# Performance work log

Hardware: AMD Instinct MI355X
Metric: run time of the kernel (lower is better)

## Reference

```python
import jax, jax.numpy as jnp
import numpy as np

U, I, D, OUT = 8192, 16384, 64, 64

def setup_inputs() -> dict:
    key = jax.random.key(0)
    k1, k2, k3, k4 = jax.random.split(key, 4)
    user_emb = jax.random.normal(k1, (U, D), dtype=jnp.float32)
    item_emb = jax.random.normal(k2, (I, D), dtype=jnp.float32)
    attention_weight = jax.random.normal(k3, (D, OUT), dtype=jnp.float32) * (1.0 / np.sqrt(D))
    adj_matrix = jax.random.randint(k4, (U, I), 0, 2, dtype=jnp.int32)
    return {"user_emb": user_emb, "item_emb": item_emb,
            "attention_weight": attention_weight, "adj_matrix": adj_matrix}

def reference(user_emb, item_emb, attention_weight, adj_matrix):
    # score[u,i] = <user_emb[u], item_emb[i]>  (torch.inner)
    score = jnp.einsum('ud,id->ui', user_emb, item_emb)
    # mask non-edges to 0 (NOT -inf, faithful to torch.where(adj>0, score, 0))
    score = jnp.where(adj_matrix > 0, score, 0.0)
    score = jax.nn.softmax(score, axis=1)
    # flag == True path: aggregate items into users, then project
    output = score @ item_emb          # [U, D]
    output = output @ attention_weight  # [U, OUT]
    return output
```

## Files before the change

### kernel.cpp

```cpp
#include <hip/hip_runtime.h>
#include <hip/hip_bf16.h>
#include <math.h>

#define U_N   8192
#define I_N   16384
#define D_N   64
#define OUT_N 64
#define BN    32
#define NCH   8
#define ITERS 64
#define VN_ST 72
#define VT_ST 40

typedef _Float16 half8  __attribute__((ext_vector_type(8)));
typedef short    bf16x8 __attribute__((ext_vector_type(8)));
typedef short    bf16x4 __attribute__((ext_vector_type(4)));
typedef float    f32x4  __attribute__((ext_vector_type(4)));
typedef int      int4v  __attribute__((ext_vector_type(4)));

static __device__ __forceinline__ unsigned short f2bf(float f) {
    union { __hip_bfloat16 h; unsigned short u; } cv;
    cv.h = __float2bfloat16(f);
    return cv.u;
}
static __device__ __forceinline__ float fast_exp2(float x) {
#if __has_builtin(__builtin_amdgcn_exp2f)
    return __builtin_amdgcn_exp2f(x);
#else
    return __expf(x * 0.6931471805599453f);
#endif
}
static __device__ __forceinline__ bf16x4 pack4(float a, float b, float c2, float d) {
    union { unsigned u[2]; bf16x4 h; } x;
#if __has_builtin(__builtin_amdgcn_perm)
    x.u[0] = __builtin_amdgcn_perm(__float_as_uint(b), __float_as_uint(a), 0x07060302u);
    x.u[1] = __builtin_amdgcn_perm(__float_as_uint(d), __float_as_uint(c2), 0x07060302u);
#else
    x.u[0] = (__float_as_uint(b) & 0xffff0000u) | (__float_as_uint(a) >> 16);
    x.u[1] = (__float_as_uint(d) & 0xffff0000u) | (__float_as_uint(c2) >> 16);
#endif
    return x.h;
}
static __device__ __forceinline__ void bar() {
    asm volatile("s_waitcnt lgkmcnt(0)\n\ts_barrier" ::: "memory");
}
static __device__ __forceinline__ f32x4 pv_mfma(bf16x4 a, bf16x4 b, f32x4 c) {
#if __has_builtin(__builtin_amdgcn_mfma_f32_16x16x16bf16_1k)
    return __builtin_amdgcn_mfma_f32_16x16x16bf16_1k(a, b, c, 0, 0, 0);
#else
    f32x4 d;
    asm volatile("v_mfma_f32_16x16x16_bf16 %0, %1, %2, %3"
                 : "=v"(d) : "v"(a), "v"(b), "v"(c));
    return d;
#endif
}

__global__ __launch_bounds__(256)
void prep_items(const float* __restrict__ item,
                _Float16* __restrict__ itemH,
                unsigned short* __restrict__ itemTt)
{
    const int i = blockIdx.x * 256 + threadIdx.x;
    const float* src = item + (size_t)i * D_N;
    f32x4 v[16];
    #pragma unroll
    for (int j = 0; j < 16; ++j) v[j] = *(const f32x4*)(src + 4 * j);

    #pragma unroll
    for (int j = 0; j < 8; ++j) {
        half8 h;
        #pragma unroll
        for (int k = 0; k < 4; ++k) { h[k] = (_Float16)v[2*j][k]; h[4+k] = (_Float16)v[2*j+1][k]; }
        *(half8*)&itemH[(size_t)i * D_N + 8 * j] = h;
    }
    const int il    = i & 31;
    const int islot = 8 * ((il & 15) >> 2) + ((il >> 4) << 2) + (il & 3);
    const size_t tb = (size_t)(i >> 5) * (D_N * 32) + islot;
    #pragma unroll
    for (int d = 0; d < 64; ++d)
        itemTt[tb + (size_t)d * 32] = f2bf(v[d >> 2][d & 3]);
}

#define DECL_SET(S) \
    int4v adj##S##a, adj##S##b; \
    half8 vn##S; bf16x8 vt##S;

#define LOAD_ADJ(S, tidx) do { \
    const size_t o_ = (size_t)(tidx) * BN; \
    adj##S##a = *(const int4v*)&adjq[o_];      \
    adj##S##b = *(const int4v*)&adjq[o_ + 16]; \
} while (0)

#define LOAD_TILE(S, tidx) do { \
    const size_t o_ = (size_t)(tidx) * BN; \
    vn##S = *(const half8*)&itemH[(ibase0 + o_ + (t >> 3)) * D_N + (t & 7) * 8]; \
    vt##S = *(const bf16x8*)&itemTt[((ibase0 + o_) >> 5) * (D_N * 32) \
                                    + (size_t)(t >> 2) * 32 + (t & 3) * 8]; \
} while (0)

#define COMMIT(S, bufw) do { \
    *(half8*)&Vn[bufw][(t >> 3) * VN_ST + (t & 7) * 8] = vn##S; \
    *(bf16x8*)&Vt[bufw][(t >> 2) * VT_ST + (t & 3) * 8] = vt##S; \
} while (0)

#define COMPUTE_REST(S, bufr) do { \
    half8 a00 = *(const half8*)&Vn[bufr][(c)      * VN_ST      + q * 8]; \
    half8 a01 = *(const half8*)&Vn[bufr][(c)      * VN_ST + 32 + q * 8]; \
    half8 a10 = *(const half8*)&Vn[bufr][(16 + c) * VN_ST      + q * 8]; \
    half8 a11 = *(const half8*)&Vn[bufr][(16 + c) * VN_ST + 32 + q * 8]; \
    bf16x8 w0 = *(const bf16x8*)&Vt[bufr][(c)      * VT_ST + 8 * q]; \
    bf16x8 w1 = *(const bf16x8*)&Vt[bufr][(16 + c) * VT_ST + 8 * q]; \
    bf16x8 w2 = *(const bf16x8*)&Vt[bufr][(32 + c) * VT_ST + 8 * q]; \
    bf16x8 w3 = *(const bf16x8*)&Vt[bufr][(48 + c) * VT_ST + 8 * q]; \
    f32x4 T0 = (f32x4){0.f,0.f,0.f,0.f}; \
    f32x4 T1 = (f32x4){0.f,0.f,0.f,0.f}; \
    T0 = __builtin_amdgcn_mfma_f32_16x16x32_f16(a00, ufrag0, T0, 0, 0, 0); \
    T0 = __builtin_amdgcn_mfma_f32_16x16x32_f16(a01, ufrag1, T0, 0, 0, 0); \
    T1 = __builtin_amdgcn_mfma_f32_16x16x32_f16(a10, ufrag0, T1, 0, 0, 0); \
    T1 = __builtin_amdgcn_mfma_f32_16x16x32_f16(a11, ufrag1, T1, 0, 0, 0); \
    const float e0_ = fast_exp2((adj##S##a[0] != 0) ? T0[0] : 0.0f); \
    const float e1_ = fast_exp2((adj##S##a[1] != 0) ? T0[1] : 0.0f); \
    const float e2_ = fast_exp2((adj##S##a[2] != 0) ? T0[2] : 0.0f); \
    const float e3_ = fast_exp2((adj##S##a[3] != 0) ? T0[3] : 0.0f); \
    const float f0_ = fast_exp2((adj##S##b[0] != 0) ? T1[0] : 0.0f); \
    const float f1_ = fast_exp2((adj##S##b[1] != 0) ? T1[1] : 0.0f); \
    const float f2_ = fast_exp2((adj##S##b[2] != 0) ? T1[2] : 0.0f); \
    const float f3_ = fast_exp2((adj##S##b[3] != 0) ? T1[3] : 0.0f); \
    lc += ((e0_ + e1_) + (e2_ + e3_)) + ((f0_ + f1_) + (f2_ + f3_)); \
    bf16x4 p0 = pack4(e0_, e1_, e2_, e3_); \
    bf16x4 p1 = pack4(f0_, f1_, f2_, f3_); \
    bf16x4 lo0 = __builtin_shufflevector(w0, w0, 0, 1, 2, 3); \
    bf16x4 hi0 = __builtin_shufflevector(w0, w0, 4, 5, 6, 7); \
    bf16x4 lo1 = __builtin_shufflevector(w1, w1, 0, 1, 2, 3); \
    bf16x4 hi1 = __builtin_shufflevector(w1, w1, 4, 5, 6, 7); \
    bf16x4 lo2 = __builtin_shufflevector(w2, w2, 0, 1, 2, 3); \
    bf16x4 hi2 = __builtin_shufflevector(w2, w2, 4, 5, 6, 7); \
    bf16x4 lo3 = __builtin_shufflevector(w3, w3, 0, 1, 2, 3); \
    bf16x4 hi3 = __builtin_shufflevector(w3, w3, 4, 5, 6, 7); \
    O0 = pv_mfma(p0, lo0, O0);  O0 = pv_mfma(p1, hi0, O0); \
    O1 = pv_mfma(p0, lo1, O1);  O1 = pv_mfma(p1, hi1, O1); \
    O2 = pv_mfma(p0, lo2, O2);  O2 = pv_mfma(p1, hi2, O2); \
    O3 = pv_mfma(p0, lo3, O3);  O3 = pv_mfma(p1, hi3, O3); \
} while (0)

__global__ __launch_bounds__(256, 4)
void atten_main(const float* __restrict__ user_emb,
                const _Float16* __restrict__ itemH,
                const unsigned short* __restrict__ itemTt,
                const int*   __restrict__ adj,
                float* __restrict__ wsO,
                float* __restrict__ wsL)
{
    __shared__ _Float16 Vn[2][BN * VN_ST];
    __shared__ short    Vt[2][D_N * VT_ST];

    const int ch   = blockIdx.x;
    const int ub   = blockIdx.y;
    const int t    = threadIdx.x;
    const int w    = t >> 6;
    const int lane = t & 63;
    const int c    = lane & 15;
    const int q    = lane >> 4;

    const int    urow0  = ub * 64 + w * 16;
    const size_t ibase0 = (size_t)ch * (I_N / NCH);

    half8 ufrag0, ufrag1;
    {
        const float* up = user_emb + (size_t)(urow0 + c) * D_N + q * 8;
        const float s = 1.44269504088896f;
        f32x4 a0 = *(const f32x4*)(up);
        f32x4 b0 = *(const f32x4*)(up + 4);
        f32x4 a1 = *(const f32x4*)(up + 32);
        f32x4 b1 = *(const f32x4*)(up + 36);
        #pragma unroll
        for (int j = 0; j < 4; ++j) {
            ufrag0[j] = (_Float16)(a0[j] * s); ufrag0[4 + j] = (_Float16)(b0[j] * s);
            ufrag1[j] = (_Float16)(a1[j] * s); ufrag1[4 + j] = (_Float16)(b1[j] * s);
        }
    }

    f32x4 O0 = (f32x4){0.f,0.f,0.f,0.f};
    f32x4 O1 = O0, O2 = O0, O3 = O0;
    float lc = 0.f;

    const int* adjq = adj + (size_t)(urow0 + c) * I_N + ibase0 + 4 * q;

    DECL_SET(A)
    DECL_SET(B)

    LOAD_TILE(A, 0); LOAD_ADJ(A, 0);
    LOAD_TILE(B, 1); LOAD_ADJ(B, 1);
    COMMIT(A, 0);
    LOAD_TILE(A, 2);
    bar();

    for (int k = 0; k < ITERS; k += 2) {
        {
            COMMIT(B, 1);
            LOAD_TILE(B, (k + 3 < ITERS) ? k + 3 : ITERS - 1);
            COMPUTE_REST(A, 0);
            LOAD_ADJ(A, (k + 2 < ITERS) ? k + 2 : ITERS - 1);
            bar();
        }
        {
            COMMIT(A, 0);
            LOAD_TILE(A, (k + 4 < ITERS) ? k + 4 : ITERS - 1);
            COMPUTE_REST(B, 1);
            LOAD_ADJ(B, (k + 3 < ITERS) ? k + 3 : ITERS - 1);
            bar();
        }
    }

    lc += __shfl_xor(lc, 16);
    lc += __shfl_xor(lc, 32);

    {
        float* d0 = wsO + ((size_t)ch * U_N + urow0 + 4 * q + 0) * D_N;
        float* d1 = wsO + ((size_t)ch * U_N + urow0 + 4 * q + 1) * D_N;
        float* d2 = wsO + ((size_t)ch * U_N + urow0 + 4 * q + 2) * D_N;
        float* d3 = wsO + ((size_t)ch * U_N + urow0 + 4 * q + 3) * D_N;
        d0[c] = O0[0]; d0[16 + c] = O1[0]; d0[32 + c] = O2[0]; d0[48 + c] = O3[0];
        d1[c] = O0[1]; d1[16 + c] = O1[1]; d1[32 + c] = O2[1]; d1[48 + c] = O3[1];
        d2[c] = O0[2]; d2[16 + c] = O1[2]; d2[32 + c] = O2[2]; d2[48 + c] = O3[2];
        d3[c] = O0[3]; d3[16 + c] = O1[3]; d3[32 + c] = O2[3]; d3[48 + c] = O3[3];
    }
    if (q == 0)
        wsL[(size_t)ch * U_N + urow0 + c] = lc;
}

__global__ __launch_bounds__(256)
void atten_combine(const float* __restrict__ wsO,
                   const float* __restrict__ wsL,
                   const float* __restrict__ attw,
                   float* __restrict__ out,
                   int nch)
{
    __shared__ float inv[64];
    __shared__ float agg[64][68];
    __shared__ float Wl[64][68];

    const int t  = threadIdx.x;
    const int u0 = blockIdx.x * 64;

    {
        const int d = t >> 2, o0 = (t & 3) * 16;
        const float* src = attw + d * OUT_N + o0;
        #pragma unroll
        for (int j = 0; j < 4; ++j)
            *(f32x4*)&Wl[d][o0 + 4 * j] = *(const f32x4*)(src + 4 * j);
    }
    if (t < 64) {
        float L = 0.f;
        for (int cc = 0; cc < nch; ++cc) L += wsL[(size_t)cc * U_N + u0 + t];
        inv[t] = 1.0f / L;
    }
    __syncthreads();

    {
        const int ul = t >> 2, d0 = (t & 3) * 16;
        const int u = u0 + ul;
        f32x4 a4[4];
        #pragma unroll
        for (int j = 0; j < 4; ++j) a4[j] = (f32x4){0.f, 0.f, 0.f, 0.f};
        for (int cc = 0; cc < nch; ++cc) {
            const float* src = wsO + ((size_t)cc * U_N + u) * D_N + d0;
            #pragma unroll
            for (int j = 0; j < 4; ++j) a4[j] += *(const f32x4*)(src + 4 * j);
        }
        const float s = inv[ul];
        #pragma unroll
        for (int j = 0; j < 4; ++j)
            *(f32x4*)&agg[ul][d0 + 4 * j] = a4[j] * s;
    }
    __syncthreads();

    {
        const int ul = t >> 2, o0 = (t & 3) * 16;
        f32x4 acc[4];
        #pragma unroll
        for (int j = 0; j < 4; ++j) acc[j] = (f32x4){0.f, 0.f, 0.f, 0.f};
        for (int d = 0; d < 64; ++d) {
            const float av = agg[ul][d];
            #pragma unroll
            for (int j = 0; j < 4; ++j) {
                f32x4 wv = *(const f32x4*)&Wl[d][o0 + 4 * j];
                acc[j] += wv * av;
            }
        }
        float* dst = out + (size_t)(u0 + ul) * OUT_N + o0;
        #pragma unroll
        for (int j = 0; j < 4; ++j)
            *(f32x4*)(dst + 4 * j) = acc[j];
    }
}

extern "C" void kernel_launch(void* const* d_in, const int* in_sizes, int n_in,
                              void* d_out, int out_size, void* d_ws, size_t ws_size,
                              hipStream_t stream)
{
    const float* user_emb = (const float*)d_in[0];
    const float* item_emb = (const float*)d_in[1];
    const float* attw     = (const float*)d_in[2];
    const int*   adj      = (const int*)d_in[3];
    float* out = (float*)d_out;

    float*          wsO    = (float*)d_ws;
    float*          wsL    = wsO + (size_t)NCH * U_N * D_N;
    _Float16*       itemH  = (_Float16*)(wsL + (size_t)NCH * U_N);
    unsigned short* itemTt = (unsigned short*)(itemH + (size_t)I_N * D_N);

    prep_items<<<dim3(I_N / 256), 256, 0, stream>>>(item_emb, itemH, itemTt);
    atten_main<<<dim3(NCH, U_N / 64), 256, 0, stream>>>(user_emb, itemH, itemTt, adj,
                                                        wsO, wsL);
    atten_combine<<<dim3(U_N / 64), 256, 0, stream>>>(wsO, wsL, attw, out, NCH);
}
```

Baseline: 728.4 us.

## Process two user row groups per wave to reuse item tiles

Each wave now handles 32 user rows (two 16-row groups 64 apart) instead of 16, so every item tile staged in shared memory feeds twice as many MFMAs and the grid halves along the user dimension. This cuts item-tile global and LDS traffic per unit of work, but raises register pressure, so the occupancy hint drops from 4 to 3 blocks per CU. The prep kernel is also split across four threads per item to reduce per-thread register use and improve parallelism. The adjacency stream, which dominates bandwidth, is unchanged.

```diff
diff --git a/kernel.cpp b/kernel.cpp
--- a/kernel.cpp
+++ b/kernel.cpp
@@ -7,6 +7,7 @@
 #define D_N   64
 #define OUT_N 64
 #define BN    32
+#define BM    128
 #define NCH   8
 #define ITERS 64
 #define VN_ST 72
@@ -60,35 +61,46 @@
                 _Float16* __restrict__ itemH,
                 unsigned short* __restrict__ itemTt)
 {
-    const int i = blockIdx.x * 256 + threadIdx.x;
-    const float* src = item + (size_t)i * D_N;
-    f32x4 v[16];
+    const int tid = blockIdx.x * 256 + threadIdx.x;
+    const int i   = tid >> 2;
+    const int g   = tid & 3;
+    const float* src = item + (size_t)i * D_N + g * 16;
+    f32x4 v0 = *(const f32x4*)(src);
+    f32x4 v1 = *(const f32x4*)(src + 4);
+    f32x4 v2 = *(const f32x4*)(src + 8);
+    f32x4 v3 = *(const f32x4*)(src + 12);
+
+    half8 h0, h1;
     #pragma unroll
-    for (int j = 0; j < 16; ++j) v[j] = *(const f32x4*)(src + 4 * j);
-
-    #pragma unroll
-    for (int j = 0; j < 8; ++j) {
-        half8 h;
-        #pragma unroll
-        for (int k = 0; k < 4; ++k) { h[k] = (_Float16)v[2*j][k]; h[4+k] = (_Float16)v[2*j+1][k]; }
-        *(half8*)&itemH[(size_t)i * D_N + 8 * j] = h;
-    }
+    for (int k = 0; k < 4; ++k) {
+        h0[k] = (_Float16)v0[k]; h0[4 + k] = (_Float16)v1[k];
+        h1[k] = (_Float16)v2[k]; h1[4 + k] = (_Float16)v3[k];
+    }
+    *(half8*)&itemH[(size_t)i * D_N + g * 16]     = h0;
+    *(half8*)&itemH[(size_t)i * D_N + g * 16 + 8] = h1;
+
     const int il    = i & 31;
     const int islot = 8 * ((il & 15) >> 2) + ((il >> 4) << 2) + (il & 3);
-    const size_t tb = (size_t)(i >> 5) * (D_N * 32) + islot;
+    unsigned short* dst = itemTt + (size_t)(i >> 5) * (D_N * 32) + (size_t)(g * 16) * 32 + islot;
     #pragma unroll
-    for (int d = 0; d < 64; ++d)
-        itemTt[tb + (size_t)d * 32] = f2bf(v[d >> 2][d & 3]);
+    for (int k = 0; k < 4; ++k) {
+        dst[(4 * 0 + k) * 32] = f2bf(v0[k]);
+        dst[(4 * 1 + k) * 32] = f2bf(v1[k]);
+        dst[(4 * 2 + k) * 32] = f2bf(v2[k]);
+        dst[(4 * 3 + k) * 32] = f2bf(v3[k]);
+    }
 }
 
 #define DECL_SET(S) \
-    int4v adj##S##a, adj##S##b; \
+    int4v adj##S##a0, adj##S##b0, adj##S##a1, adj##S##b1; \
     half8 vn##S; bf16x8 vt##S;
 
 #define LOAD_ADJ(S, tidx) do { \
     const size_t o_ = (size_t)(tidx) * BN; \
-    adj##S##a = *(const int4v*)&adjq[o_];      \
-    adj##S##b = *(const int4v*)&adjq[o_ + 16]; \
+    adj##S##a0 = *(const int4v*)&adjq0[o_];      \
+    adj##S##b0 = *(const int4v*)&adjq0[o_ + 16]; \
+    adj##S##a1 = *(const int4v*)&adjq1[o_];      \
+    adj##S##b1 = *(const int4v*)&adjq1[o_ + 16]; \
 } while (0)
 
 #define LOAD_TILE(S, tidx) do { \
@@ -113,22 +125,37 @@
     bf16x8 w2 = *(const bf16x8*)&Vt[bufr][(32 + c) * VT_ST + 8 * q]; \
     bf16x8 w3 = *(const bf16x8*)&Vt[bufr][(48 + c) * VT_ST + 8 * q]; \
     f32x4 T0 = (f32x4){0.f,0.f,0.f,0.f}; \
-    f32x4 T1 = (f32x4){0.f,0.f,0.f,0.f}; \
+    f32x4 T1 = T0, T2 = T0, T3 = T0; \
     T0 = __builtin_amdgcn_mfma_f32_16x16x32_f16(a00, ufrag0, T0, 0, 0, 0); \
+    T2 = __builtin_amdgcn_mfma_f32_16x16x32_f16(a00, ufrag2, T2, 0, 0, 0); \
     T0 = __builtin_amdgcn_mfma_f32_16x16x32_f16(a01, ufrag1, T0, 0, 0, 0); \
+    T2 = __builtin_amdgcn_mfma_f32_16x16x32_f16(a01, ufrag3, T2, 0, 0, 0); \
     T1 = __builtin_amdgcn_mfma_f32_16x16x32_f16(a10, ufrag0, T1, 0, 0, 0); \
+    T3 = __builtin_amdgcn_mfma_f32_16x16x32_f16(a10, ufrag2, T3, 0, 0, 0); \
     T1 = __builtin_amdgcn_mfma_f32_16x16x32_f16(a11, ufrag1, T1, 0, 0, 0); \
-    const float e0_ = fast_exp2((adj##S##a[0] != 0) ? T0[0] : 0.0f); \
-    const float e1_ = fast_exp2((adj##S##a[1] != 0) ? T0[1] : 0.0f); \
-    const float e2_ = fast_exp2((adj##S##a[2] != 0) ? T0[2] : 0.0f); \
-    const float e3_ = fast_exp2((adj##S##a[3] != 0) ? T0[3] : 0.0f); \
-    const float f0_ = fast_exp2((adj##S##b[0] != 0) ? T1[0] : 0.0f); \
-    const float f1_ = fast_exp2((adj##S##b[1] != 0) ? T1[1] : 0.0f); \
-    const float f2_ = fast_exp2((adj##S##b[2] != 0) ? T1[2] : 0.0f); \
-    const float f3_ = fast_exp2((adj##S##b[3] != 0) ? T1[3] : 0.0f); \
-    lc += ((e0_ + e1_) + (e2_ + e3_)) + ((f0_ + f1_) + (f2_ + f3_)); \
+    T3 = __builtin_amdgcn_mfma_f32_16x16x32_f16(a11, ufrag3, T3, 0, 0, 0); \
+    const float e0_ = fast_exp2((adj##S##a0[0] != 0) ? T0[0] : 0.0f); \
+    const float e1_ = fast_exp2((adj##S##a0[1] != 0) ? T0[1] : 0.0f); \
+    const float e2_ = fast_exp2((adj##S##a0[2] != 0) ? T0[2] : 0.0f); \
+    const float e3_ = fast_exp2((adj##S##a0[3] != 0) ? T0[3] : 0.0f); \
+    const float f0_ = fast_exp2((adj##S##b0[0] != 0) ? T1[0] : 0.0f); \
+    const float f1_ = fast_exp2((adj##S##b0[1] != 0) ? T1[1] : 0.0f); \
+    const float f2_ = fast_exp2((adj##S##b0[2] != 0) ? T1[2] : 0.0f); \
+    const float f3_ = fast_exp2((adj##S##b0[3] != 0) ? T1[3] : 0.0f); \
+    const float g0_ = fast_exp2((adj##S##a1[0] != 0) ? T2[0] : 0.0f); \
+    const float g1_ = fast_exp2((adj##S##a1[1] != 0) ? T2[1] : 0.0f); \
+    const float g2_ = fast_exp2((adj##S##a1[2] != 0) ? T2[2] : 0.0f); \
+    const float g3_ = fast_exp2((adj##S##a1[3] != 0) ? T2[3] : 0.0f); \
+    const float h0_ = fast_exp2((adj##S##b1[0] != 0) ? T3[0] : 0.0f); \
+    const float h1_ = fast_exp2((adj##S##b1[1] != 0) ? T3[1] : 0.0f); \
+    const float h2_ = fast_exp2((adj##S##b1[2] != 0) ? T3[2] : 0.0f); \
+    const float h3_ = fast_exp2((adj##S##b1[3] != 0) ? T3[3] : 0.0f); \
+    lc0 += ((e0_ + e1_) + (e2_ + e3_)) + ((f0_ + f1_) + (f2_ + f3_)); \
+    lc1 += ((g0_ + g1_) + (g2_ + g3_)) + ((h0_ + h1_) + (h2_ + h3_)); \
     bf16x4 p0 = pack4(e0_, e1_, e2_, e3_); \
     bf16x4 p1 = pack4(f0_, f1_, f2_, f3_); \
+    bf16x4 p2 = pack4(g0_, g1_, g2_, g3_); \
+    bf16x4 p3 = pack4(h0_, h1_, h2_, h3_); \
     bf16x4 lo0 = __builtin_shufflevector(w0, w0, 0, 1, 2, 3); \
     bf16x4 hi0 = __builtin_shufflevector(w0, w0, 4, 5, 6, 7); \
     bf16x4 lo1 = __builtin_shufflevector(w1, w1, 0, 1, 2, 3); \
@@ -137,13 +164,17 @@
     bf16x4 hi2 = __builtin_shufflevector(w2, w2, 4, 5, 6, 7); \
     bf16x4 lo3 = __builtin_shufflevector(w3, w3, 0, 1, 2, 3); \
     bf16x4 hi3 = __builtin_shufflevector(w3, w3, 4, 5, 6, 7); \
-    O0 = pv_mfma(p0, lo0, O0);  O0 = pv_mfma(p1, hi0, O0); \
-    O1 = pv_mfma(p0, lo1, O1);  O1 = pv_mfma(p1, hi1, O1); \
-    O2 = pv_mfma(p0, lo2, O2);  O2 = pv_mfma(p1, hi2, O2); \
-    O3 = pv_mfma(p0, lo3, O3);  O3 = pv_mfma(p1, hi3, O3); \
+    O0 = pv_mfma(p0, lo0, O0);  O4 = pv_mfma(p2, lo0, O4); \
+    O0 = pv_mfma(p1, hi0, O0);  O4 = pv_mfma(p3, hi0, O4); \
+    O1 = pv_mfma(p0, lo1, O1);  O5 = pv_mfma(p2, lo1, O5); \
+    O1 = pv_mfma(p1, hi1, O1);  O5 = pv_mfma(p3, hi1, O5); \
+    O2 = pv_mfma(p0, lo2, O2);  O6 = pv_mfma(p2, lo2, O6); \
+    O2 = pv_mfma(p1, hi2, O2);  O6 = pv_mfma(p3, hi2, O6); \
+    O3 = pv_mfma(p0, lo3, O3);  O7 = pv_mfma(p2, lo3, O7); \
+    O3 = pv_mfma(p1, hi3, O3);  O7 = pv_mfma(p3, hi3, O7); \
 } while (0)
 
-__global__ __launch_bounds__(256, 4)
+__global__ __launch_bounds__(256, 3)
 void atten_main(const float* __restrict__ user_emb,
                 const _Float16* __restrict__ itemH,
                 const unsigned short* __restrict__ itemTt,
@@ -162,29 +193,37 @@
     const int c    = lane & 15;
     const int q    = lane >> 4;
 
-    const int    urow0  = ub * 64 + w * 16;
+    const int    urow0  = ub * BM + w * 16;
     const size_t ibase0 = (size_t)ch * (I_N / NCH);
 
-    half8 ufrag0, ufrag1;
-    {
-        const float* up = user_emb + (size_t)(urow0 + c) * D_N + q * 8;
+    half8 ufrag0, ufrag1, ufrag2, ufrag3;
+    {
         const float s = 1.44269504088896f;
-        f32x4 a0 = *(const f32x4*)(up);
-        f32x4 b0 = *(const f32x4*)(up + 4);
-        f32x4 a1 = *(const f32x4*)(up + 32);
-        f32x4 b1 = *(const f32x4*)(up + 36);
+        const float* up0 = user_emb + (size_t)(urow0 + c) * D_N + q * 8;
+        const float* up1 = up0 + (size_t)64 * D_N;
+        f32x4 a0 = *(const f32x4*)(up0);
+        f32x4 b0 = *(const f32x4*)(up0 + 4);
+        f32x4 a1 = *(const f32x4*)(up0 + 32);
+        f32x4 b1 = *(const f32x4*)(up0 + 36);
+        f32x4 a2 = *(const f32x4*)(up1);
+        f32x4 b2 = *(const f32x4*)(up1 + 4);
+        f32x4 a3 = *(const f32x4*)(up1 + 32);
+        f32x4 b3 = *(const f32x4*)(up1 + 36);
         #pragma unroll
         for (int j = 0; j < 4; ++j) {
             ufrag0[j] = (_Float16)(a0[j] * s); ufrag0[4 + j] = (_Float16)(b0[j] * s);
             ufrag1[j] = (_Float16)(a1[j] * s); ufrag1[4 + j] = (_Float16)(b1[j] * s);
+            ufrag2[j] = (_Float16)(a2[j] * s); ufrag2[4 + j] = (_Float16)(b2[j] * s);
+            ufrag3[j] = (_Float16)(a3[j] * s); ufrag3[4 + j] = (_Float16)(b3[j] * s);
         }
     }
 
     f32x4 O0 = (f32x4){0.f,0.f,0.f,0.f};
-    f32x4 O1 = O0, O2 = O0, O3 = O0;
-    float lc = 0.f;
-
-    const int* adjq = adj + (size_t)(urow0 + c) * I_N + ibase0 + 4 * q;
+    f32x4 O1 = O0, O2 = O0, O3 = O0, O4 = O0, O5 = O0, O6 = O0, O7 = O0;
+    float lc0 = 0.f, lc1 = 0.f;
+
+    const int* adjq0 = adj + (size_t)(urow0 + c) * I_N + ibase0 + 4 * q;
+    const int* adjq1 = adjq0 + (size_t)64 * I_N;
 
     DECL_SET(A)
     DECL_SET(B)
@@ -212,8 +251,10 @@
         }
     }
 
-    lc += __shfl_xor(lc, 16);
-    lc += __shfl_xor(lc, 32);
+    lc0 += __shfl_xor(lc0, 16);
+    lc0 += __shfl_xor(lc0, 32);
+    lc1 += __shfl_xor(lc1, 16);
+    lc1 += __shfl_xor(lc1, 32);
 
     {
         float* d0 = wsO + ((size_t)ch * U_N + urow0 + 4 * q + 0) * D_N;
@@ -224,9 +265,19 @@
         d1[c] = O0[1]; d1[16 + c] = O1[1]; d1[32 + c] = O2[1]; d1[48 + c] = O3[1];
         d2[c] = O0[2]; d2[16 + c] = O1[2]; d2[32 + c] = O2[2]; d2[48 + c] = O3[2];
         d3[c] = O0[3]; d3[16 + c] = O1[3]; d3[32 + c] = O2[3]; d3[48 + c] = O3[3];
-    }
-    if (q == 0)
-        wsL[(size_t)ch * U_N + urow0 + c] = lc;
+        float* e0 = d0 + (size_t)64 * D_N;
+        float* e1 = d1 + (size_t)64 * D_N;
+        float* e2 = d2 + (size_t)64 * D_N;
+        float* e3 = d3 + (size_t)64 * D_N;
+        e0[c] = O4[0]; e0[16 + c] = O5[0]; e0[32 + c] = O6[0]; e0[48 + c] = O7[0];
+        e1[c] = O4[1]; e1[16 + c] = O5[1]; e1[32 + c] = O6[1]; e1[48 + c] = O7[1];
+        e2[c] = O4[2]; e2[16 + c] = O5[2]; e2[32 + c] = O6[2]; e2[48 + c] = O7[2];
+        e3[c] = O4[3]; e3[16 + c] = O5[3]; e3[32 + c] = O6[3]; e3[48 + c] = O7[3];
+    }
+    if (q == 0) {
+        wsL[(size_t)ch * U_N + urow0 + c]      = lc0;
+        wsL[(size_t)ch * U_N + urow0 + 64 + c] = lc1;
+    }
 }
 
 __global__ __launch_bounds__(256)
@@ -310,8 +361,8 @@
     _Float16*       itemH  = (_Float16*)(wsL + (size_t)NCH * U_N);
     unsigned short* itemTt = (unsigned short*)(itemH + (size_t)I_N * D_N);
 
-    prep_items<<<dim3(I_N / 256), 256, 0, stream>>>(item_emb, itemH, itemTt);
-    atten_main<<<dim3(NCH, U_N / 64), 256, 0, stream>>>(user_emb, itemH, itemTt, adj,
+    prep_items<<<dim3(I_N * 4 / 256), 256, 0, stream>>>(item_emb, itemH, itemTt);
+    atten_main<<<dim3(NCH, U_N / BM), 256, 0, stream>>>(user_emb, itemH, itemTt, adj,
                                                         wsO, wsL);
     atten_combine<<<dim3(U_N / 64), 256, 0, stream>>>(wsO, wsL, attw, out, NCH);
 }
```

Result: no change. 736.2 us (+1.1%).
